# Kernel tuning notes

Hardware: AMD Instinct MI355X
Metric: run time of the kernel (lower is better)

Reference implementation:

```python
import jax, jax.numpy as jnp
import numpy as np

D_MODEL = 1024
H = 16
DK = 64  # d_model // h
M = 8    # memory slots
NQ = 1024
B = 8


def setup_inputs() -> dict:
    key = jax.random.key(0)
    ks = jax.random.split(key, 10)
    f = lambda k, s, sc=1.0: jax.random.normal(k, s, dtype=jnp.float32) * sc
    return {
        "queries": f(ks[0], (NQ, B, D_MODEL)),
        "keys": f(ks[1], (NQ, B, D_MODEL)),
        "values": f(ks[2], (NQ, B, D_MODEL)),
        "m_k": f(ks[3], (1, M, D_MODEL), 0.1),
        "m_v": f(ks[4], (1, M, D_MODEL), 0.1),
        "attn_mask": f(ks[5], (B, H, NQ, NQ), 0.02),  # additive float mask over real keys
        "in_proj_weight": f(ks[6], (3 * D_MODEL, D_MODEL), 0.02),
        "in_proj_bias": jnp.zeros((3 * D_MODEL,), jnp.float32),
        "out_w": f(ks[7], (D_MODEL, D_MODEL), 0.02),
        "out_b": jnp.zeros((D_MODEL,), jnp.float32),
    }


def _fp16(w):
    # The torch module casts projection weights/biases to fp16 before linear.
    return w.astype(jnp.float16).astype(jnp.float32)


def reference(queries, keys, values, m_k, m_v, attn_mask,
              in_proj_weight, in_proj_bias, out_w, out_b):
    # (seq, batch, d) -> (batch, seq, d)
    q_in = queries.transpose(1, 0, 2)
    k_in = keys.transpose(1, 0, 2)
    v_in = values.transpose(1, 0, 2)
    b, nq, d = q_in.shape
    nk = k_in.shape[1]
    m = m_k.shape[1]

    w_q, w_k, w_v = jnp.split(in_proj_weight, 3, axis=0)
    b_q, b_k, b_v = jnp.split(in_proj_bias, 3)

    q = q_in @ _fp16(w_q).T + _fp16(b_q)
    k = k_in @ _fp16(w_k).T + _fp16(b_k)
    v = v_in @ _fp16(w_v).T + _fp16(b_v)

    # scaled learnable memory slots, broadcast over batch
    mk = float(np.sqrt(DK * H)) * jnp.broadcast_to(m_k, (b, m, d))
    mv = float(np.sqrt(m)) * jnp.broadcast_to(m_v, (b, m, d))
    k = jnp.concatenate([k, mk], axis=1)  # (b, nk+m, d)
    v = jnp.concatenate([v, mv], axis=1)

    qh = q.reshape(b, nq, H, DK).transpose(0, 2, 1, 3)        # (b,h,nq,dk)
    kh = k.reshape(b, nk + m, H, DK).transpose(0, 2, 3, 1)    # (b,h,dk,nk+m)
    vh = v.reshape(b, nk + m, H, DK).transpose(0, 2, 1, 3)    # (b,h,nk+m,dv)

    att = jnp.matmul(qh, kh) / float(np.sqrt(DK))             # (b,h,nq,nk+m)
    # additive mask applies only to the real keys, memory slots unmasked
    mask_pad = jnp.concatenate(
        [attn_mask, jnp.zeros((b, H, nq, m), att.dtype)], axis=-1)
    att = jax.nn.softmax(att + mask_pad, axis=-1)

    out = jnp.matmul(att, vh).transpose(0, 2, 1, 3).reshape(b, nq, H * DK)
    out = out @ out_w.T + out_b
    return out.transpose(1, 0, 2)  # back to (seq, batch, d)
```

## Files before the change

kernel.cpp:

```cpp
#include <hip/hip_runtime.h>
#include <cstdint>

typedef _Float16 half8  __attribute__((ext_vector_type(8)));
typedef _Float16 half4v __attribute__((ext_vector_type(4)));
typedef float    f32x4  __attribute__((ext_vector_type(4)));

#define MFMA_F16(a,b,c) __builtin_amdgcn_mfma_f32_16x16x32_f16(a,b,c,0,0,0)

static constexpr int D = 1024, H = 16, DK = 64, BATCH = 8, NQ = 1024;
static constexpr int NKP = 1040;

__global__ __launch_bounds__(256) void gemm_qkv(
    const float* __restrict__ Aq, const float* __restrict__ Ak, const float* __restrict__ Av,
    const float* __restrict__ W, const float* __restrict__ bias,
    _Float16* __restrict__ Qo, _Float16* __restrict__ Ko, _Float16* __restrict__ Vo)
{
  const int z = blockIdx.z;
  const float* __restrict__ A = (z == 0) ? Aq : ((z == 1) ? Ak : Av);
  const int row0 = blockIdx.x * 128;
  const int col0 = blockIdx.y * 128;
  const float* __restrict__ Wz = W + (size_t)z * D * D;

  __shared__ _Float16 As[128 * 40];
  __shared__ _Float16 Bs[128 * 40];

  const int tid = threadIdx.x;
  const int wv = tid >> 6, lane = tid & 63, c = lane & 15, g = lane >> 4;
  const int ar0 = (wv & 1) * 64, bc0 = (wv >> 1) * 64;

  f32x4 acc[4][4];
#pragma unroll
  for (int i = 0; i < 4; i++)
#pragma unroll
    for (int j = 0; j < 4; j++) acc[i][j] = (f32x4)(0.f);

  for (int kb = 0; kb < D; kb += 32) {
#pragma unroll
    for (int u = 0; u < 2; u++) {
      int id = tid + 256 * u;
      int row = id >> 2, k8 = (id & 3) * 8;
      const float* ap = A + (size_t)(row0 + row) * D + kb + k8;
      float4 f0 = ((const float4*)ap)[0];
      float4 f1 = ((const float4*)ap)[1];
      half8 ha;
      ha[0]=(_Float16)f0.x; ha[1]=(_Float16)f0.y; ha[2]=(_Float16)f0.z; ha[3]=(_Float16)f0.w;
      ha[4]=(_Float16)f1.x; ha[5]=(_Float16)f1.y; ha[6]=(_Float16)f1.z; ha[7]=(_Float16)f1.w;
      *(half8*)&As[row * 40 + k8] = ha;

      const float* wp = Wz + (size_t)(col0 + row) * D + kb + k8;
      float4 g0 = ((const float4*)wp)[0];
      float4 g1 = ((const float4*)wp)[1];
      half8 hb;
      hb[0]=(_Float16)g0.x; hb[1]=(_Float16)g0.y; hb[2]=(_Float16)g0.z; hb[3]=(_Float16)g0.w;
      hb[4]=(_Float16)g1.x; hb[5]=(_Float16)g1.y; hb[6]=(_Float16)g1.z; hb[7]=(_Float16)g1.w;
      *(half8*)&Bs[row * 40 + k8] = hb;
    }
    __syncthreads();
    half8 af[4], bf[4];
#pragma unroll
    for (int i = 0; i < 4; i++) af[i] = *(const half8*)&As[(ar0 + 16 * i + c) * 40 + 8 * g];
#pragma unroll
    for (int j = 0; j < 4; j++) bf[j] = *(const half8*)&Bs[(bc0 + 16 * j + c) * 40 + 8 * g];
#pragma unroll
    for (int i = 0; i < 4; i++)
#pragma unroll
      for (int j = 0; j < 4; j++) acc[i][j] = MFMA_F16(af[i], bf[j], acc[i][j]);
    __syncthreads();
  }

#pragma unroll
  for (int j = 0; j < 4; j++) {
    int n = col0 + bc0 + 16 * j + c;
    float bb = (float)(_Float16)bias[z * D + n];
    int h_ = n >> 6, dk = n & 63;
#pragma unroll
    for (int i = 0; i < 4; i++) {
#pragma unroll
      for (int r = 0; r < 4; r++) {
        int m = row0 + ar0 + 16 * i + 4 * g + r;
        int b = m & 7, nq = m >> 3;
        float val = acc[i][j][r] + bb;
        if (z == 0)
          Qo[(((size_t)b * H + h_) * NQ + nq) * DK + dk] = (_Float16)(val * 0.125f);
        else if (z == 1)
          Ko[(((size_t)b * H + h_) * NKP + nq) * DK + dk] = (_Float16)val;
        else
          Vo[(((size_t)b * H + h_) * NKP + nq) * DK + dk] = (_Float16)val;
      }
    }
  }
}

__global__ __launch_bounds__(256) void fill_slots(
    const float* __restrict__ mk, const float* __restrict__ mv,
    _Float16* __restrict__ Ko, _Float16* __restrict__ Vo)
{
  int idx = blockIdx.x * 256 + threadIdx.x;
  int which = idx >> 17;
  int e = idx & 131071;
  int dk = e & 63, r = (e >> 6) & 15, h = (e >> 10) & 15, b = (e >> 14) & 7;
  float val = 0.f;
  if (r < 8) {
    int src = r * D + h * DK + dk;
    val = which ? 2.8284271247461903f * mv[src] : 32.f * mk[src];
  }
  _Float16* dst = which ? Vo : Ko;
  dst[(((size_t)b * H + h) * NKP + 1024 + r) * DK + dk] = (_Float16)val;
}

__global__ __launch_bounds__(256) void attn(
    const _Float16* __restrict__ Qg, const _Float16* __restrict__ Kg,
    const _Float16* __restrict__ Vg, const float* __restrict__ mask,
    _Float16* __restrict__ Hid)
{
  const int qt = blockIdx.x;
  const int bh = blockIdx.y;
  const int b = bh >> 4, h = bh & 15;
  const int tid = threadIdx.x;
  const int wv = tid >> 6, lane = tid & 63, c = lane & 15, g = lane >> 4;

  __shared__ _Float16 Qs[64 * 72];
  __shared__ _Float16 Ks[64 * 72];
  __shared__ _Float16 Vt[64 * 72];
  __shared__ _Float16 Ps[64 * 72];

  const _Float16* qbase = Qg + ((size_t)bh * NQ + qt * 64) * DK;
#pragma unroll
  for (int u = 0; u < 2; u++) {
    int id = tid + 256 * u;
    int row = id >> 3, m8 = (id & 7) * 8;
    *(int4*)&Qs[row * 72 + m8] = *(const int4*)(qbase + row * DK + m8);
  }
  __syncthreads();
  const int qrow = (wv * 16 + c) * 72;
  half8 qf0 = *(const half8*)&Qs[qrow + 8 * g];
  half8 qf1 = *(const half8*)&Qs[qrow + 32 + 8 * g];

  f32x4 oacc[4];
#pragma unroll
  for (int j = 0; j < 4; j++) oacc[j] = (f32x4)(0.f);
  float lpart = 0.f;

  const float* maskbase = mask + ((size_t)bh << 20) + ((size_t)(qt * 64 + wv * 16 + c) << 10);
  const _Float16* kbase_g = Kg + (size_t)bh * NKP * DK;
  const _Float16* vbase_g = Vg + (size_t)bh * NKP * DK;

  for (int ci = 0; ci < 17; ++ci) {
    const int kb = ci * 64;
    const int nk = (ci < 16) ? 64 : 16;
    __syncthreads();

    f32x4 sinit[4];
    if (ci < 16) {
#pragma unroll
      for (int t = 0; t < 4; t++)
        sinit[t] = *(const f32x4*)(maskbase + kb + 16 * t + 4 * g);
    } else {
      float iv = (g < 2) ? 0.f : -1e30f;
      sinit[0] = (f32x4){iv, iv, iv, iv};
    }

#pragma unroll
    for (int u = 0; u < 2; u++) {
      int id = tid + 256 * u;
      int row = id >> 3, m8 = (id & 7) * 8;
      if (row < nk)
        *(int4*)&Ks[row * 72 + m8] = *(const int4*)(kbase_g + (size_t)(kb + row) * DK + m8);
    }
    {
      int kp = tid & 31, dvo = (tid >> 5) * 8;
      if (2 * kp < nk) {
        uint4 a4 = *(const uint4*)(vbase_g + (size_t)(kb + 2 * kp) * DK + dvo);
        uint4 b4 = *(const uint4*)(vbase_g + (size_t)(kb + 2 * kp + 1) * DK + dvo);
        uint32_t aw[4] = {a4.x, a4.y, a4.z, a4.w};
        uint32_t bw[4] = {b4.x, b4.y, b4.z, b4.w};
#pragma unroll
        for (int w = 0; w < 4; w++) {
          uint32_t lo = (aw[w] & 0xffffu) | (bw[w] << 16);
          uint32_t hi = (aw[w] >> 16) | (bw[w] & 0xffff0000u);
          *(uint32_t*)&Vt[(dvo + 2 * w) * 72 + 2 * kp] = lo;
          *(uint32_t*)&Vt[(dvo + 2 * w + 1) * 72 + 2 * kp] = hi;
        }
      } else if (nk == 16) {
#pragma unroll
        for (int w = 0; w < 4; w++) {
          *(uint32_t*)&Vt[(dvo + 2 * w) * 72 + 2 * kp] = 0u;
          *(uint32_t*)&Vt[(dvo + 2 * w + 1) * 72 + 2 * kp] = 0u;
        }
      }
    }
    __syncthreads();

    const int ntile = nk >> 4;
    for (int t = 0; t < ntile; ++t) {
      f32x4 s = sinit[t];
      half8 kf0 = *(const half8*)&Ks[(16 * t + c) * 72 + 8 * g];
      half8 kf1 = *(const half8*)&Ks[(16 * t + c) * 72 + 32 + 8 * g];
      s = MFMA_F16(kf0, qf0, s);
      s = MFMA_F16(kf1, qf1, s);
      f32x4 p;
      p[0] = __expf(s[0]); p[1] = __expf(s[1]); p[2] = __expf(s[2]); p[3] = __expf(s[3]);
      lpart += p[0] + p[1] + p[2] + p[3];
      half4v ph;
      ph[0] = (_Float16)p[0]; ph[1] = (_Float16)p[1];
      ph[2] = (_Float16)p[2]; ph[3] = (_Float16)p[3];
      *(half4v*)&Ps[qrow + 16 * t + 4 * g] = ph;
    }
    if (nk == 16) {
      half4v zz = {(_Float16)0, (_Float16)0, (_Float16)0, (_Float16)0};
      *(half4v*)&Ps[qrow + 16 + 4 * g] = zz;
    }

    const int khalf = (nk == 64) ? 2 : 1;
    for (int kh = 0; kh < khalf; ++kh) {
      half8 pf = *(const half8*)&Ps[qrow + 32 * kh + 8 * g];
#pragma unroll
      for (int j = 0; j < 4; j++) {
        half8 vf = *(const half8*)&Vt[(16 * j + c) * 72 + 32 * kh + 8 * g];
        oacc[j] = MFMA_F16(pf, vf, oacc[j]);
      }
    }
  }

  lpart += __shfl_xor(lpart, 16);
  lpart += __shfl_xor(lpart, 32);
  float inv_[4];
#pragma unroll
  for (int r = 0; r < 4; r++) {
    float lq = __shfl(lpart, 4 * g + r);
    inv_[r] = __builtin_amdgcn_rcpf(lq);
  }
#pragma unroll
  for (int j = 0; j < 4; j++) {
    int col = h * DK + 16 * j + c;
#pragma unroll
    for (int r = 0; r < 4; r++) {
      int q = qt * 64 + wv * 16 + 4 * g + r;
      Hid[((size_t)q * BATCH + b) * D + col] = (_Float16)(oacc[j][r] * inv_[r]);
    }
  }
}

__global__ __launch_bounds__(256) void gemm_out(
    const _Float16* __restrict__ Ah, const float* __restrict__ W,
    const float* __restrict__ bias, float* __restrict__ Out)
{
  const int row0 = blockIdx.x * 128, col0 = blockIdx.y * 128;
  __shared__ _Float16 As[128 * 40];
  __shared__ _Float16 Bs[128 * 40];
  const int tid = threadIdx.x;
  const int wv = tid >> 6, lane = tid & 63, c = lane & 15, g = lane >> 4;
  const int ar0 = (wv & 1) * 64, bc0 = (wv >> 1) * 64;

  f32x4 acc[4][4];
#pragma unroll
  for (int i = 0; i < 4; i++)
#pragma unroll
    for (int j = 0; j < 4; j++) acc[i][j] = (f32x4)(0.f);

  for (int kb = 0; kb < D; kb += 32) {
#pragma unroll
    for (int u = 0; u < 2; u++) {
      int id = tid + 256 * u;
      int row = id >> 2, k8 = (id & 3) * 8;
      *(int4*)&As[row * 40 + k8] =
          *(const int4*)(Ah + (size_t)(row0 + row) * D + kb + k8);
      const float* wp = W + (size_t)(col0 + row) * D + kb + k8;
      float4 g0 = ((const float4*)wp)[0];
      float4 g1 = ((const float4*)wp)[1];
      half8 hb;
      hb[0]=(_Float16)g0.x; hb[1]=(_Float16)g0.y; hb[2]=(_Float16)g0.z; hb[3]=(_Float16)g0.w;
      hb[4]=(_Float16)g1.x; hb[5]=(_Float16)g1.y; hb[6]=(_Float16)g1.z; hb[7]=(_Float16)g1.w;
      *(half8*)&Bs[row * 40 + k8] = hb;
    }
    __syncthreads();
    half8 af[4], bf[4];
#pragma unroll
    for (int i = 0; i < 4; i++) af[i] = *(const half8*)&As[(ar0 + 16 * i + c) * 40 + 8 * g];
#pragma unroll
    for (int j = 0; j < 4; j++) bf[j] = *(const half8*)&Bs[(bc0 + 16 * j + c) * 40 + 8 * g];
#pragma unroll
    for (int i = 0; i < 4; i++)
#pragma unroll
      for (int j = 0; j < 4; j++) acc[i][j] = MFMA_F16(af[i], bf[j], acc[i][j]);
    __syncthreads();
  }

#pragma unroll
  for (int j = 0; j < 4; j++) {
    int n = col0 + bc0 + 16 * j + c;
    float bb = bias[n];
#pragma unroll
    for (int i = 0; i < 4; i++) {
#pragma unroll
      for (int r = 0; r < 4; r++) {
        int m = row0 + ar0 + 16 * i + 4 * g + r;
        Out[(size_t)m * D + n] = acc[i][j][r] + bb;
      }
    }
  }
}

extern "C" void kernel_launch(void* const* d_in, const int* in_sizes, int n_in,
                              void* d_out, int out_size, void* d_ws, size_t ws_size,
                              hipStream_t stream) {
  const float* queries   = (const float*)d_in[0];
  const float* keys      = (const float*)d_in[1];
  const float* values    = (const float*)d_in[2];
  const float* m_k       = (const float*)d_in[3];
  const float* m_v       = (const float*)d_in[4];
  const float* attn_mask = (const float*)d_in[5];
  const float* in_proj_w = (const float*)d_in[6];
  const float* in_proj_b = (const float*)d_in[7];
  const float* out_w     = (const float*)d_in[8];
  const float* out_b     = (const float*)d_in[9];
  float* out = (float*)d_out;

  _Float16* Qw = (_Float16*)d_ws;
  _Float16* Kw = Qw + (size_t)8 * 16 * 1024 * 64;
  _Float16* Vw = Kw + (size_t)8 * 16 * 1040 * 64;
  _Float16* Hw = Vw + (size_t)8 * 16 * 1040 * 64;

  hipLaunchKernelGGL(gemm_qkv, dim3(64, 8, 3), dim3(256), 0, stream,
                     queries, keys, values, in_proj_w, in_proj_b, Qw, Kw, Vw);
  hipLaunchKernelGGL(fill_slots, dim3(1024), dim3(256), 0, stream, m_k, m_v, Kw, Vw);
  hipLaunchKernelGGL(attn, dim3(16, 128), dim3(256), 0, stream, Qw, Kw, Vw, attn_mask, Hw);
  hipLaunchKernelGGL(gemm_out, dim3(64, 8), dim3(256), 0, stream, Hw, out_w, out_b, out);
}
```

Measured before the change: 963.5 us.

## Pre-convert inputs and weights to fp16 and stream GEMM tiles via direct-to-LDS loads

```diff
diff --git a/kernel.cpp b/kernel.cpp
--- a/kernel.cpp
+++ b/kernel.cpp
@@ -10,24 +10,64 @@
 static constexpr int D = 1024, H = 16, DK = 64, BATCH = 8, NQ = 1024;
 static constexpr int NKP = 1040;
 
+__device__ __forceinline__ void async_copy16(_Float16* lds, const _Float16* g) {
+  __builtin_amdgcn_global_load_lds(
+      (const __attribute__((address_space(1))) void*)g,
+      (__attribute__((address_space(3))) void*)lds, 16, 0, 0);
+}
+
+__global__ __launch_bounds__(256) void convert_all(
+    const float* __restrict__ q, const float* __restrict__ k, const float* __restrict__ v,
+    const float* __restrict__ w_in, const float* __restrict__ w_out,
+    _Float16* __restrict__ q16, _Float16* __restrict__ k16, _Float16* __restrict__ v16,
+    _Float16* __restrict__ win16, _Float16* __restrict__ wout16)
+{
+  const unsigned NA = 8192u * 1024u;
+  const unsigned NW = 3u * 1024u * 1024u;
+  unsigned idx = blockIdx.x * 256u + threadIdx.x;
+  unsigned e = idx * 8u;
+  const float* src;
+  _Float16* dst;
+  unsigned off;
+  if (e < NA)            { src = q;     dst = q16;    off = e; }
+  else if (e < 2 * NA)   { src = k;     dst = k16;    off = e - NA; }
+  else if (e < 3 * NA)   { src = v;     dst = v16;    off = e - 2 * NA; }
+  else if (e < 3 * NA + NW) { src = w_in; dst = win16; off = e - 3 * NA; }
+  else                   { src = w_out; dst = wout16; off = e - 3 * NA - NW; }
+  float4 f0 = ((const float4*)(src + off))[0];
+  float4 f1 = ((const float4*)(src + off))[1];
+  half8 h;
+  h[0]=(_Float16)f0.x; h[1]=(_Float16)f0.y; h[2]=(_Float16)f0.z; h[3]=(_Float16)f0.w;
+  h[4]=(_Float16)f1.x; h[5]=(_Float16)f1.y; h[6]=(_Float16)f1.z; h[7]=(_Float16)f1.w;
+  *(half8*)(dst + off) = h;
+}
+
 __global__ __launch_bounds__(256) void gemm_qkv(
-    const float* __restrict__ Aq, const float* __restrict__ Ak, const float* __restrict__ Av,
-    const float* __restrict__ W, const float* __restrict__ bias,
+    const _Float16* __restrict__ A16,
+    const _Float16* __restrict__ W16,
+    const float* __restrict__ bias,
     _Float16* __restrict__ Qo, _Float16* __restrict__ Ko, _Float16* __restrict__ Vo)
 {
   const int z = blockIdx.z;
-  const float* __restrict__ A = (z == 0) ? Aq : ((z == 1) ? Ak : Av);
+  const _Float16* __restrict__ A = A16 + (size_t)z * 8192 * 1024;
+  const _Float16* __restrict__ Wz = W16 + (size_t)z * D * D;
   const int row0 = blockIdx.x * 128;
   const int col0 = blockIdx.y * 128;
-  const float* __restrict__ Wz = W + (size_t)z * D * D;
-
-  __shared__ _Float16 As[128 * 40];
-  __shared__ _Float16 Bs[128 * 40];
+
+  __shared__ _Float16 As[128 * 32];
+  __shared__ _Float16 Bs[128 * 32];
 
   const int tid = threadIdx.x;
   const int wv = tid >> 6, lane = tid & 63, c = lane & 15, g = lane >> 4;
   const int ar0 = (wv & 1) * 64, bc0 = (wv >> 1) * 64;
 
+  const int srow = 32 * wv + (lane >> 2);
+  const int sk8 = (lane & 3) * 8;
+  const _Float16* ag = A + (size_t)(row0 + srow) * D + sk8;
+  const _Float16* bg = Wz + (size_t)(col0 + srow) * D + sk8;
+  _Float16* al = &As[(32 * wv) * 32];
+  _Float16* bl = &Bs[(32 * wv) * 32];
+
   f32x4 acc[4][4];
 #pragma unroll
   for (int i = 0; i < 4; i++)
@@ -35,32 +75,16 @@
     for (int j = 0; j < 4; j++) acc[i][j] = (f32x4)(0.f);
 
   for (int kb = 0; kb < D; kb += 32) {
-#pragma unroll
-    for (int u = 0; u < 2; u++) {
-      int id = tid + 256 * u;
-      int row = id >> 2, k8 = (id & 3) * 8;
-      const float* ap = A + (size_t)(row0 + row) * D + kb + k8;
-      float4 f0 = ((const float4*)ap)[0];
-      float4 f1 = ((const float4*)ap)[1];
-      half8 ha;
-      ha[0]=(_Float16)f0.x; ha[1]=(_Float16)f0.y; ha[2]=(_Float16)f0.z; ha[3]=(_Float16)f0.w;
-      ha[4]=(_Float16)f1.x; ha[5]=(_Float16)f1.y; ha[6]=(_Float16)f1.z; ha[7]=(_Float16)f1.w;
-      *(half8*)&As[row * 40 + k8] = ha;
-
-      const float* wp = Wz + (size_t)(col0 + row) * D + kb + k8;
-      float4 g0 = ((const float4*)wp)[0];
-      float4 g1 = ((const float4*)wp)[1];
-      half8 hb;
-      hb[0]=(_Float16)g0.x; hb[1]=(_Float16)g0.y; hb[2]=(_Float16)g0.z; hb[3]=(_Float16)g0.w;
-      hb[4]=(_Float16)g1.x; hb[5]=(_Float16)g1.y; hb[6]=(_Float16)g1.z; hb[7]=(_Float16)g1.w;
-      *(half8*)&Bs[row * 40 + k8] = hb;
-    }
+    async_copy16(al,           ag + kb);
+    async_copy16(al + 16 * 32, ag + kb + (size_t)16 * D);
+    async_copy16(bl,           bg + kb);
+    async_copy16(bl + 16 * 32, bg + kb + (size_t)16 * D);
     __syncthreads();
     half8 af[4], bf[4];
 #pragma unroll
-    for (int i = 0; i < 4; i++) af[i] = *(const half8*)&As[(ar0 + 16 * i + c) * 40 + 8 * g];
-#pragma unroll
-    for (int j = 0; j < 4; j++) bf[j] = *(const half8*)&Bs[(bc0 + 16 * j + c) * 40 + 8 * g];
+    for (int i = 0; i < 4; i++) af[i] = *(const half8*)&As[(ar0 + 16 * i + c) * 32 + 8 * g];
+#pragma unroll
+    for (int j = 0; j < 4; j++) bf[j] = *(const half8*)&Bs[(bc0 + 16 * j + c) * 32 + 8 * g];
 #pragma unroll
     for (int i = 0; i < 4; i++)
 #pragma unroll
@@ -242,16 +266,23 @@
 }
 
 __global__ __launch_bounds__(256) void gemm_out(
-    const _Float16* __restrict__ Ah, const float* __restrict__ W,
+    const _Float16* __restrict__ Ah, const _Float16* __restrict__ W16,
     const float* __restrict__ bias, float* __restrict__ Out)
 {
   const int row0 = blockIdx.x * 128, col0 = blockIdx.y * 128;
-  __shared__ _Float16 As[128 * 40];
-  __shared__ _Float16 Bs[128 * 40];
+  __shared__ _Float16 As[128 * 32];
+  __shared__ _Float16 Bs[128 * 32];
   const int tid = threadIdx.x;
   const int wv = tid >> 6, lane = tid & 63, c = lane & 15, g = lane >> 4;
   const int ar0 = (wv & 1) * 64, bc0 = (wv >> 1) * 64;
 
+  const int srow = 32 * wv + (lane >> 2);
+  const int sk8 = (lane & 3) * 8;
+  const _Float16* ag = Ah + (size_t)(row0 + srow) * D + sk8;
+  const _Float16* bg = W16 + (size_t)(col0 + srow) * D + sk8;
+  _Float16* al = &As[(32 * wv) * 32];
+  _Float16* bl = &Bs[(32 * wv) * 32];
+
   f32x4 acc[4][4];
 #pragma unroll
   for (int i = 0; i < 4; i++)
@@ -259,26 +290,16 @@
     for (int j = 0; j < 4; j++) acc[i][j] = (f32x4)(0.f);
 
   for (int kb = 0; kb < D; kb += 32) {
-#pragma unroll
-    for (int u = 0; u < 2; u++) {
-      int id = tid + 256 * u;
-      int row = id >> 2, k8 = (id & 3) * 8;
-      *(int4*)&As[row * 40 + k8] =
-          *(const int4*)(Ah + (size_t)(row0 + row) * D + kb + k8);
-      const float* wp = W + (size_t)(col0 + row) * D + kb + k8;
-      float4 g0 = ((const float4*)wp)[0];
-      float4 g1 = ((const float4*)wp)[1];
-      half8 hb;
-      hb[0]=(_Float16)g0.x; hb[1]=(_Float16)g0.y; hb[2]=(_Float16)g0.z; hb[3]=(_Float16)g0.w;
-      hb[4]=(_Float16)g1.x; hb[5]=(_Float16)g1.y; hb[6]=(_Float16)g1.z; hb[7]=(_Float16)g1.w;
-      *(half8*)&Bs[row * 40 + k8] = hb;
-    }
+    async_copy16(al,           ag + kb);
+    async_copy16(al + 16 * 32, ag + kb + (size_t)16 * D);
+    async_copy16(bl,           bg + kb);
+    async_copy16(bl + 16 * 32, bg + kb + (size_t)16 * D);
     __syncthreads();
     half8 af[4], bf[4];
 #pragma unroll
-    for (int i = 0; i < 4; i++) af[i] = *(const half8*)&As[(ar0 + 16 * i + c) * 40 + 8 * g];
-#pragma unroll
-    for (int j = 0; j < 4; j++) bf[j] = *(const half8*)&Bs[(bc0 + 16 * j + c) * 40 + 8 * g];
+    for (int i = 0; i < 4; i++) af[i] = *(const half8*)&As[(ar0 + 16 * i + c) * 32 + 8 * g];
+#pragma unroll
+    for (int j = 0; j < 4; j++) bf[j] = *(const half8*)&Bs[(bc0 + 16 * j + c) * 32 + 8 * g];
 #pragma unroll
     for (int i = 0; i < 4; i++)
 #pragma unroll
@@ -316,14 +337,21 @@
   const float* out_b     = (const float*)d_in[9];
   float* out = (float*)d_out;
 
-  _Float16* Qw = (_Float16*)d_ws;
+  const size_t NA = (size_t)8192 * 1024;
+  _Float16* A16  = (_Float16*)d_ws;
+  _Float16* Win16  = A16 + 3 * NA;
+  _Float16* Wout16 = Win16 + (size_t)3 * 1024 * 1024;
+  _Float16* Qw = Wout16 + (size_t)1024 * 1024;
   _Float16* Kw = Qw + (size_t)8 * 16 * 1024 * 64;
   _Float16* Vw = Kw + (size_t)8 * 16 * 1040 * 64;
   _Float16* Hw = Vw + (size_t)8 * 16 * 1040 * 64;
 
+  hipLaunchKernelGGL(convert_all, dim3(14336), dim3(256), 0, stream,
+                     queries, keys, values, in_proj_w, out_w,
+                     A16, A16 + NA, A16 + 2 * NA, Win16, Wout16);
   hipLaunchKernelGGL(gemm_qkv, dim3(64, 8, 3), dim3(256), 0, stream,
-                     queries, keys, values, in_proj_w, in_proj_b, Qw, Kw, Vw);
+                     A16, Win16, in_proj_b, Qw, Kw, Vw);
   hipLaunchKernelGGL(fill_slots, dim3(1024), dim3(256), 0, stream, m_k, m_v, Kw, Vw);
   hipLaunchKernelGGL(attn, dim3(16, 128), dim3(256), 0, stream, Qw, Kw, Vw, attn_mask, Hw);
-  hipLaunchKernelGGL(gemm_out, dim3(64, 8), dim3(256), 0, stream, Hw, out_w, out_b, out);
-}
+  hipLaunchKernelGGL(gemm_out, dim3(64, 8), dim3(256), 0, stream, Hw, Wout16, out_b, out);
+}
```

Result: no change. 948.6 us (-1.5%).
